# Kernel optimization log

Hardware: AMD Instinct MI355X
Metric: run time of the kernel (lower is better)

Reference implementation:

```python
import jax, jax.numpy as jnp
import numpy as np
from jax.ops import segment_sum

N_NODES = 100_000
N_EDGES = 3_200_000
IN_DIM = 128
HID1, HID2, OUT = 32, 16, 1
N_GRAPHS = 512


def gcn_conv(x, src, dst, W, b, n_nodes):
    """PyG GCNConv: add self-loops, symmetric deg^{-1/2} norm, scatter-add, bias."""
    h = x @ W  # [N, out]
    loop = jnp.arange(n_nodes, dtype=src.dtype)
    s = jnp.concatenate([src, loop])
    d = jnp.concatenate([dst, loop])
    deg = segment_sum(jnp.ones_like(d, dtype=h.dtype), d, num_segments=n_nodes)
    dinv = jax.lax.rsqrt(jnp.maximum(deg, 1.0))  # deg >= 1 due to self-loops
    norm = dinv[s] * dinv[d]  # [E+N]
    msg = h[s] * norm[:, None]  # gather + scale
    out = segment_sum(msg, d, num_segments=n_nodes)  # scatter-add to dst
    return out + b


def setup_inputs() -> dict:
    key = jax.random.key(0)
    ks = jax.random.split(key, 9)
    x = jax.random.normal(ks[0], (N_NODES, IN_DIM), dtype=jnp.float32)
    edge_index = jax.random.randint(ks[1], (2, N_EDGES), 0, N_NODES, dtype=jnp.int64)
    batch = jnp.sort(jax.random.randint(ks[2], (N_NODES,), 0, N_GRAPHS, dtype=jnp.int64))
    W1 = jax.random.normal(ks[3], (IN_DIM, HID1), dtype=jnp.float32) * 0.1
    b1 = jnp.zeros((HID1,), dtype=jnp.float32)
    W2 = jax.random.normal(ks[4], (HID1, HID2), dtype=jnp.float32) * 0.1
    b2 = jnp.zeros((HID2,), dtype=jnp.float32)
    W3 = jax.random.normal(ks[5], (HID2, OUT), dtype=jnp.float32) * 0.1
    b3 = jnp.zeros((OUT,), dtype=jnp.float32)
    return {"x": x, "edge_index": edge_index, "batch": batch,
            "W1": W1, "b1": b1, "W2": W2, "b2": b2, "W3": W3, "b3": b3}


def reference(x, edge_index, batch, W1, b1, W2, b2, W3, b3):
    src, dst = edge_index[0], edge_index[1]
    n = x.shape[0]
    h = jax.nn.relu(gcn_conv(x, src, dst, W1, b1, n))
    h = jax.nn.relu(gcn_conv(h, src, dst, W2, b2, n))
    # global_mean_pool: segment mean over graph ids
    summed = segment_sum(h, batch, num_segments=N_GRAPHS)  # [G, HID2]
    counts = segment_sum(jnp.ones((n,), dtype=h.dtype), batch, num_segments=N_GRAPHS)
    pooled = summed / jnp.maximum(counts, 1.0)[:, None]
    return pooled @ W3 + b3  # [G, 1]
```

## Files before the change

kernel.cpp:

```cpp
#include <hip/hip_runtime.h>
#include <hip/hip_fp16.h>

#define NN 100000
#define NE 3200000
#define NG 512
#define IND 128
#define H1D 32
#define H2D 16
#define BSH 7
#define BN  128
#define NB  782
#define TILE 8192
#define CAP 5120

#define O_DINV   0u
#define O_ROW    100352u
#define O_REND   200704u
#define O_GCUR   301056u
#define O_GSUM   302080u
#define O_M1H    302592u
#define O_M2H    1902592u
#define O_CSRB   2702592u
#define O_CSR    6706432u

__global__ __launch_bounds__(256) void k_init(int* gcur, float* gsum) {
    int i = blockIdx.x * 256 + threadIdx.x;
    if (i < 1024) gcur[i] = i * CAP;
    if (i < NG) gsum[i] = 0.f;
}

__global__ __launch_bounds__(256) void k_binfill(const int* __restrict__ src,
                                                 const int* __restrict__ dst,
                                                 int* __restrict__ gcur,
                                                 unsigned* __restrict__ csrb) {
    __shared__ unsigned se[TILE];
    __shared__ int lc[NB], lofs[NB], lcur[NB], gb[NB];
    __shared__ int sp[256];
    int t = threadIdx.x;
    for (int i = t; i < NB; i += 256) lc[i] = 0;
    __syncthreads();
    int base = blockIdx.x * TILE;
    int end = min(base + TILE, NE);
    int n4 = (end - base) >> 2;
    const int4* dst4 = (const int4*)(dst + base);
    const int4* src4 = (const int4*)(src + base);
    for (int u = t; u < n4; u += 256) {
        int4 v = dst4[u];
        atomicAdd(&lc[v.x >> BSH], 1);
        atomicAdd(&lc[v.y >> BSH], 1);
        atomicAdd(&lc[v.z >> BSH], 1);
        atomicAdd(&lc[v.w >> BSH], 1);
    }
    __syncthreads();
    int b0 = 4 * t;
    int c0 = (b0     < NB) ? lc[b0]     : 0;
    int c1 = (b0 + 1 < NB) ? lc[b0 + 1] : 0;
    int c2 = (b0 + 2 < NB) ? lc[b0 + 2] : 0;
    int c3 = (b0 + 3 < NB) ? lc[b0 + 3] : 0;
    int s4 = c0 + c1 + c2 + c3;
    sp[t] = s4;
    __syncthreads();
    for (int off = 1; off < 256; off <<= 1) {
        int v = (t >= off) ? sp[t - off] : 0;
        __syncthreads();
        sp[t] += v;
        __syncthreads();
    }
    int excl = sp[t] - s4;
    if (b0     < NB) { lofs[b0]     = excl;               lcur[b0]     = excl; }
    if (b0 + 1 < NB) { lofs[b0 + 1] = excl + c0;          lcur[b0 + 1] = excl + c0; }
    if (b0 + 2 < NB) { lofs[b0 + 2] = excl + c0 + c1;     lcur[b0 + 2] = excl + c0 + c1; }
    if (b0 + 3 < NB) { lofs[b0 + 3] = excl + c0 + c1 + c2; lcur[b0 + 3] = excl + c0 + c1 + c2; }
    __syncthreads();
    for (int i = t; i < NB; i += 256) {
        int c = lc[i];
        gb[i] = c ? atomicAdd(&gcur[i], c) : 0;
    }
    __syncthreads();
    for (int u = t; u < n4; u += 256) {
        int4 vd = dst4[u];
        int4 vs = src4[u];
        int b, p;
        b = vd.x >> BSH; p = atomicAdd(&lcur[b], 1);
        se[p] = (unsigned)vs.x | ((unsigned)(vd.x & (BN - 1)) << 17);
        b = vd.y >> BSH; p = atomicAdd(&lcur[b], 1);
        se[p] = (unsigned)vs.y | ((unsigned)(vd.y & (BN - 1)) << 17);
        b = vd.z >> BSH; p = atomicAdd(&lcur[b], 1);
        se[p] = (unsigned)vs.z | ((unsigned)(vd.z & (BN - 1)) << 17);
        b = vd.w >> BSH; p = atomicAdd(&lcur[b], 1);
        se[p] = (unsigned)vs.w | ((unsigned)(vd.w & (BN - 1)) << 17);
    }
    __syncthreads();
    int wv = t >> 6, ln = t & 63;
    for (int b = wv; b < NB; b += 4) {
        int cnt = lc[b];
        int lo = lofs[b], g = gb[b];
        for (int u = ln; u < cnt; u += 64)
            csrb[g + u] = se[lo + u];
    }
}

__global__ __launch_bounds__(256) void k_reorder(const unsigned* __restrict__ csrb,
                                                 const int* __restrict__ gcur,
                                                 int* __restrict__ rowstart,
                                                 int* __restrict__ rowend,
                                                 float* __restrict__ dinv,
                                                 int* __restrict__ csr) {
    __shared__ unsigned se[CAP];
    __shared__ unsigned so[CAP];
    __shared__ int h[BN], cur[BN];
    int t = threadIdx.x;
    int b = blockIdx.x;
    int base = b * CAP;
    int cnt = gcur[b] - base;
    if (t < BN) h[t] = 0;
    __syncthreads();
    for (int i = t; i < cnt; i += 256) {
        unsigned p = csrb[base + i];
        se[i] = p;
        atomicAdd(&h[p >> 17], 1);
    }
    __syncthreads();
    int deg = (t < BN) ? h[t] : 0;
    for (int off = 1; off < BN; off <<= 1) {
        int v = (t < BN && t >= off) ? h[t - off] : 0;
        __syncthreads();
        if (t < BN) h[t] += v;
        __syncthreads();
    }
    int excl = (t < BN) ? (h[t] - deg) : 0;
    if (t < BN) cur[t] = excl;
    int node = (b << BSH) + t;
    if (t < BN && node < NN) {
        rowstart[node] = base + excl;
        rowend[node]   = base + excl + deg;
        dinv[node] = 1.0f / sqrtf((float)(deg + 1));
    }
    __syncthreads();
    for (int i = t; i < cnt; i += 256) {
        unsigned p = se[i];
        int pos = atomicAdd(&cur[p >> 17], 1);
        so[pos] = p;
    }
    __syncthreads();
    for (int i = t; i < cnt; i += 256)
        csr[base + i] = (int)(so[i] & 0x1FFFF);
}

__global__ __launch_bounds__(256) void k_gemm1(const float* __restrict__ x,
                                               const float* __restrict__ W1,
                                               const float* __restrict__ dinv,
                                               __half* __restrict__ m1h) {
    __shared__ float sWt[32 * 132];
    __shared__ float sX[16 * IND];
    int t = threadIdx.x;
    for (int idx = t; idx < IND * H1D; idx += 256) {
        int i = idx >> 5, k = idx & 31;
        sWt[k * 132 + i] = W1[idx];
    }
    const float4* x4 = (const float4*)(x + (size_t)blockIdx.x * 16 * IND);
    ((float4*)sX)[t] = x4[t];
    ((float4*)sX)[t + 256] = x4[t + 256];
    __syncthreads();
    int r = t >> 5, k = t & 31;
    float a0 = 0.f, a1 = 0.f;
#pragma unroll
    for (int i = 0; i < IND; i += 4) {
        float4 w = *(const float4*)&sWt[k * 132 + i];
        float4 p = *(const float4*)&sX[r * IND + i];
        float4 s = *(const float4*)&sX[(r + 8) * IND + i];
        a0 += p.x * w.x + p.y * w.y + p.z * w.z + p.w * w.w;
        a1 += s.x * w.x + s.y * w.y + s.z * w.z + s.w * w.w;
    }
    int n0 = blockIdx.x * 16 + r;
    m1h[(size_t)n0 * 32 + k] = __float2half(a0 * dinv[n0]);
    m1h[(size_t)(n0 + 8) * 32 + k] = __float2half(a1 * dinv[n0 + 8]);
}

__device__ __forceinline__ void h8_acc(const float4& r, float* a) {
    const __half2* h = (const __half2*)&r;
    float2 f0 = __half22float2(h[0]);
    float2 f1 = __half22float2(h[1]);
    float2 f2 = __half22float2(h[2]);
    float2 f3 = __half22float2(h[3]);
    a[0] += f0.x; a[1] += f0.y; a[2] += f1.x; a[3] += f1.y;
    a[4] += f2.x; a[5] += f2.y; a[6] += f3.x; a[7] += f3.y;
}

__global__ __launch_bounds__(256) void k_agg1(const __half* __restrict__ m1h,
                                              const float* __restrict__ dinv,
                                              const int* __restrict__ rowstart,
                                              const int* __restrict__ rowend,
                                              const int* __restrict__ csr,
                                              const float* __restrict__ b1,
                                              const float* __restrict__ W2,
                                              __half* __restrict__ m2h) {
    int t = threadIdx.x;
    int lane = t & 63;
    int j = (lane >> 2) & 7;
    int q = lane & 3;
    int d = (blockIdx.x * 256 + t) >> 5;
    int beg = rowstart[d], end = rowend[d];
    float dv = dinv[d];
    const float4* m4 = (const float4*)m1h;
    float4 selfr = m4[(size_t)d * 4 + q];
    float a[8] = {0.f, 0.f, 0.f, 0.f, 0.f, 0.f, 0.f, 0.f};
    int i = beg + j;
    for (; i + 24 < end; i += 32) {
        int s0 = csr[i], s1 = csr[i + 8], s2 = csr[i + 16], s3 = csr[i + 24];
        float4 A = m4[(size_t)s0 * 4 + q];
        float4 B = m4[(size_t)s1 * 4 + q];
        float4 C = m4[(size_t)s2 * 4 + q];
        float4 D = m4[(size_t)s3 * 4 + q];
        h8_acc(A, a); h8_acc(B, a); h8_acc(C, a); h8_acc(D, a);
    }
    for (; i + 8 < end; i += 16) {
        int s0 = csr[i], s1 = csr[i + 8];
        float4 A = m4[(size_t)s0 * 4 + q];
        float4 B = m4[(size_t)s1 * 4 + q];
        h8_acc(A, a); h8_acc(B, a);
    }
    if (i < end) {
        int s0 = csr[i];
        float4 A = m4[(size_t)s0 * 4 + q];
        h8_acc(A, a);
    }
#pragma unroll
    for (int m = 4; m <= 16; m <<= 1) {
#pragma unroll
        for (int e = 0; e < 8; ++e) a[e] += __shfl_xor(a[e], m);
    }
    float sf[8] = {0.f, 0.f, 0.f, 0.f, 0.f, 0.f, 0.f, 0.f};
    h8_acc(selfr, sf);
    float4 ba = ((const float4*)b1)[q * 2];
    float4 bb = ((const float4*)b1)[q * 2 + 1];
    float bias[8] = {ba.x, ba.y, ba.z, ba.w, bb.x, bb.y, bb.z, bb.w};
    float v[8];
#pragma unroll
    for (int e = 0; e < 8; ++e)
        v[e] = fmaxf((a[e] + sf[e]) * dv + bias[e], 0.f);
    const float2* W2_2 = (const float2*)W2;
    float p0 = 0.f, p1 = 0.f;
#pragma unroll
    for (int e = 0; e < 8; ++e) {
        float2 w = W2_2[(q * 8 + e) * 8 + j];
        p0 += v[e] * w.x;
        p1 += v[e] * w.y;
    }
    p0 += __shfl_xor(p0, 1); p1 += __shfl_xor(p1, 1);
    p0 += __shfl_xor(p0, 2); p1 += __shfl_xor(p1, 2);
    if (q == 0)
        *(__half2*)&m2h[(size_t)d * 16 + 2 * j] = __floats2half2_rn(p0 * dv, p1 * dv);
}

__global__ __launch_bounds__(256) void k_agg2(const __half* __restrict__ m2h,
                                              const float* __restrict__ dinv,
                                              const int* __restrict__ rowstart,
                                              const int* __restrict__ rowend,
                                              const int* __restrict__ csr,
                                              const float* __restrict__ b2,
                                              const float* __restrict__ W3,
                                              const int* __restrict__ batch,
                                              float* __restrict__ gsum) {
    __shared__ float bsum[8];
    __shared__ int   bg[8];
    int t = threadIdx.x;
    int lane = t & 63;
    int j = (lane >> 1) & 15;
    int q = lane & 1;
    int d = (blockIdx.x * 256 + t) >> 5;
    int beg = rowstart[d], end = rowend[d];
    float dv = dinv[d];
    const float4* m4 = (const float4*)m2h;
    float4 selfr = m4[(size_t)d * 2 + q];
    float a[8] = {0.f, 0.f, 0.f, 0.f, 0.f, 0.f, 0.f, 0.f};
    int i = beg + j;
    for (; i + 48 < end; i += 64) {
        int s0 = csr[i], s1 = csr[i + 16], s2 = csr[i + 32], s3 = csr[i + 48];
        float4 A = m4[(size_t)s0 * 2 + q];
        float4 B = m4[(size_t)s1 * 2 + q];
        float4 C = m4[(size_t)s2 * 2 + q];
        float4 D = m4[(size_t)s3 * 2 + q];
        h8_acc(A, a); h8_acc(B, a); h8_acc(C, a); h8_acc(D, a);
    }
    for (; i + 16 < end; i += 32) {
        int s0 = csr[i], s1 = csr[i + 16];
        float4 A = m4[(size_t)s0 * 2 + q];
        float4 B = m4[(size_t)s1 * 2 + q];
        h8_acc(A, a); h8_acc(B, a);
    }
    if (i < end) {
        int s0 = csr[i];
        float4 A = m4[(size_t)s0 * 2 + q];
        h8_acc(A, a);
    }
#pragma unroll
    for (int m = 2; m <= 16; m <<= 1) {
#pragma unroll
        for (int e = 0; e < 8; ++e) a[e] += __shfl_xor(a[e], m);
    }
    float sf[8] = {0.f, 0.f, 0.f, 0.f, 0.f, 0.f, 0.f, 0.f};
    h8_acc(selfr, sf);
    float4 ba = ((const float4*)b2)[q * 2];
    float4 bb = ((const float4*)b2)[q * 2 + 1];
    float4 wa = ((const float4*)W3)[q * 2];
    float4 wb = ((const float4*)W3)[q * 2 + 1];
    float bias[8] = {ba.x, ba.y, ba.z, ba.w, bb.x, bb.y, bb.z, bb.w};
    float w3[8]   = {wa.x, wa.y, wa.z, wa.w, wb.x, wb.y, wb.z, wb.w};
    float partial = 0.f;
#pragma unroll
    for (int e = 0; e < 8; ++e) {
        float v = fmaxf((a[e] + sf[e]) * dv + bias[e], 0.f);
        partial += v * w3[e];
    }
    partial += __shfl_xor(partial, 1);
    int hw = t >> 5;
    if ((lane & 31) == 0) { bg[hw] = batch[d]; bsum[hw] = partial; }
    __syncthreads();
    if (t == 0) {
        float s = bsum[0]; int g = bg[0];
#pragma unroll
        for (int u = 1; u < 8; ++u) {
            if (bg[u] == g) s += bsum[u];
            else { atomicAdd(&gsum[g], s); g = bg[u]; s = bsum[u]; }
        }
        atomicAdd(&gsum[g], s);
    }
}

__global__ __launch_bounds__(256) void k_final(const float* __restrict__ gsum,
                                               const int* __restrict__ batch,
                                               const float* __restrict__ b3,
                                               float* __restrict__ out) {
    int g = blockIdx.x * 256 + threadIdx.x;
    if (g >= NG) return;
    int lo = 0, hi = NN;
    while (lo < hi) { int mid = (lo + hi) >> 1; if (batch[mid] < g) lo = mid + 1; else hi = mid; }
    int lo2 = lo, hi2 = NN;
    while (lo2 < hi2) { int mid = (lo2 + hi2) >> 1; if (batch[mid] < g + 1) lo2 = mid + 1; else hi2 = mid; }
    out[g] = gsum[g] / fmaxf((float)(lo2 - lo), 1.0f) + b3[0];
}

extern "C" void kernel_launch(void* const* d_in, const int* in_sizes, int n_in,
                              void* d_out, int out_size, void* d_ws, size_t ws_size,
                              hipStream_t stream) {
    const float* x     = (const float*)d_in[0];
    const int*   src   = (const int*)d_in[1];
    const int*   dst   = src + NE;
    const int*   batch = (const int*)d_in[2];
    const float* W1 = (const float*)d_in[3];
    const float* b1 = (const float*)d_in[4];
    const float* W2 = (const float*)d_in[5];
    const float* b2 = (const float*)d_in[6];
    const float* W3 = (const float*)d_in[7];
    const float* b3 = (const float*)d_in[8];
    float* out = (float*)d_out;

    float* ws = (float*)d_ws;
    float*    dinv     = ws + O_DINV;
    int*      rowstart = (int*)(ws + O_ROW);
    int*      rowend   = (int*)(ws + O_REND);
    int*      gcur     = (int*)(ws + O_GCUR);
    float*    gsum     = ws + O_GSUM;
    __half*   m1h      = (__half*)(ws + O_M1H);
    __half*   m2h      = (__half*)(ws + O_M2H);
    unsigned* csrb     = (unsigned*)(ws + O_CSRB);
    int*      csr      = (int*)(ws + O_CSR);

    k_init   <<<4, 256, 0, stream>>>(gcur, gsum);
    k_binfill<<<(NE + TILE - 1) / TILE, 256, 0, stream>>>(src, dst, gcur, csrb);
    k_reorder<<<NB, 256, 0, stream>>>(csrb, gcur, rowstart, rowend, dinv, csr);

    k_gemm1  <<<NN / 16, 256, 0, stream>>>(x, W1, dinv, m1h);
    k_agg1   <<<NN / 8, 256, 0, stream>>>(m1h, dinv, rowstart, rowend, csr, b1, W2, m2h);
    k_agg2   <<<NN / 8, 256, 0, stream>>>(m2h, dinv, rowstart, rowend, csr, b2, W3, batch, gsum);
    k_final  <<<2, 256, 0, stream>>>(gsum, batch, b3, out);
}
```

Measured before the change: 324.4 us.

## Merge edge binning and first GEMM into one heterogeneous launch; defer dinv scaling

Edge binning and the x@W1 GEMM now run as two groups of blocks inside a single launch, so the GEMM no longer waits for the degree computation. The dinv scaling of m1h moves into the reorder kernel as an in-place half2 pass. The binning tile stores 16-bit local edge indices in shared memory instead of packed 32-bit entries and re-reads src/dst from global when writing out. The reorder kernel drops its shared staging buffer and reads csrb twice from global. The cost is an extra read-modify-write of m1h and extra global reads in exchange for one fewer launch and cross-stage overlap.

```diff
diff --git a/kernel.cpp b/kernel.cpp
--- a/kernel.cpp
+++ b/kernel.cpp
@@ -11,6 +11,7 @@
 #define BN  128
 #define NB  782
 #define TILE 8192
+#define NBF 391
 #define CAP 5120
 
 #define O_DINV   0u
@@ -29,74 +30,105 @@
     if (i < NG) gsum[i] = 0.f;
 }
 
-__global__ __launch_bounds__(256) void k_binfill(const int* __restrict__ src,
-                                                 const int* __restrict__ dst,
-                                                 int* __restrict__ gcur,
-                                                 unsigned* __restrict__ csrb) {
-    __shared__ unsigned se[TILE];
-    __shared__ int lc[NB], lofs[NB], lcur[NB], gb[NB];
-    __shared__ int sp[256];
+__global__ __launch_bounds__(256) void k_prep1(const int* __restrict__ src,
+                                               const int* __restrict__ dst,
+                                               int* __restrict__ gcur,
+                                               unsigned* __restrict__ csrb,
+                                               const float* __restrict__ x,
+                                               const float* __restrict__ W1,
+                                               __half* __restrict__ m1h) {
+    __shared__ __align__(16) unsigned char smem[30208];
     int t = threadIdx.x;
-    for (int i = t; i < NB; i += 256) lc[i] = 0;
-    __syncthreads();
-    int base = blockIdx.x * TILE;
-    int end = min(base + TILE, NE);
-    int n4 = (end - base) >> 2;
-    const int4* dst4 = (const int4*)(dst + base);
-    const int4* src4 = (const int4*)(src + base);
-    for (int u = t; u < n4; u += 256) {
-        int4 v = dst4[u];
-        atomicAdd(&lc[v.x >> BSH], 1);
-        atomicAdd(&lc[v.y >> BSH], 1);
-        atomicAdd(&lc[v.z >> BSH], 1);
-        atomicAdd(&lc[v.w >> BSH], 1);
-    }
-    __syncthreads();
-    int b0 = 4 * t;
-    int c0 = (b0     < NB) ? lc[b0]     : 0;
-    int c1 = (b0 + 1 < NB) ? lc[b0 + 1] : 0;
-    int c2 = (b0 + 2 < NB) ? lc[b0 + 2] : 0;
-    int c3 = (b0 + 3 < NB) ? lc[b0 + 3] : 0;
-    int s4 = c0 + c1 + c2 + c3;
-    sp[t] = s4;
-    __syncthreads();
-    for (int off = 1; off < 256; off <<= 1) {
-        int v = (t >= off) ? sp[t - off] : 0;
-        __syncthreads();
-        sp[t] += v;
-        __syncthreads();
-    }
-    int excl = sp[t] - s4;
-    if (b0     < NB) { lofs[b0]     = excl;               lcur[b0]     = excl; }
-    if (b0 + 1 < NB) { lofs[b0 + 1] = excl + c0;          lcur[b0 + 1] = excl + c0; }
-    if (b0 + 2 < NB) { lofs[b0 + 2] = excl + c0 + c1;     lcur[b0 + 2] = excl + c0 + c1; }
-    if (b0 + 3 < NB) { lofs[b0 + 3] = excl + c0 + c1 + c2; lcur[b0 + 3] = excl + c0 + c1 + c2; }
-    __syncthreads();
-    for (int i = t; i < NB; i += 256) {
-        int c = lc[i];
-        gb[i] = c ? atomicAdd(&gcur[i], c) : 0;
-    }
-    __syncthreads();
-    for (int u = t; u < n4; u += 256) {
-        int4 vd = dst4[u];
-        int4 vs = src4[u];
-        int b, p;
-        b = vd.x >> BSH; p = atomicAdd(&lcur[b], 1);
-        se[p] = (unsigned)vs.x | ((unsigned)(vd.x & (BN - 1)) << 17);
-        b = vd.y >> BSH; p = atomicAdd(&lcur[b], 1);
-        se[p] = (unsigned)vs.y | ((unsigned)(vd.y & (BN - 1)) << 17);
-        b = vd.z >> BSH; p = atomicAdd(&lcur[b], 1);
-        se[p] = (unsigned)vs.z | ((unsigned)(vd.z & (BN - 1)) << 17);
-        b = vd.w >> BSH; p = atomicAdd(&lcur[b], 1);
-        se[p] = (unsigned)vs.w | ((unsigned)(vd.w & (BN - 1)) << 17);
-    }
-    __syncthreads();
-    int wv = t >> 6, ln = t & 63;
-    for (int b = wv; b < NB; b += 4) {
-        int cnt = lc[b];
-        int lo = lofs[b], g = gb[b];
-        for (int u = ln; u < cnt; u += 64)
-            csrb[g + u] = se[lo + u];
+    if (blockIdx.x < NBF) {
+        unsigned short* se16 = (unsigned short*)smem;
+        int* lc   = (int*)(smem + 16384);
+        int* lofs = (int*)(smem + 19584);
+        int* lcur = (int*)(smem + 22784);
+        int* gb   = (int*)(smem + 25984);
+        int* sp   = (int*)(smem + 29184);
+        for (int i = t; i < NB; i += 256) lc[i] = 0;
+        __syncthreads();
+        int base = blockIdx.x * TILE;
+        int end = min(base + TILE, NE);
+        int n = end - base;
+        int n4 = n >> 2;
+        const int4* dst4 = (const int4*)(dst + base);
+        for (int u = t; u < n4; u += 256) {
+            int4 v = dst4[u];
+            atomicAdd(&lc[v.x >> BSH], 1);
+            atomicAdd(&lc[v.y >> BSH], 1);
+            atomicAdd(&lc[v.z >> BSH], 1);
+            atomicAdd(&lc[v.w >> BSH], 1);
+        }
+        __syncthreads();
+        int b0 = 4 * t;
+        int c0 = (b0     < NB) ? lc[b0]     : 0;
+        int c1 = (b0 + 1 < NB) ? lc[b0 + 1] : 0;
+        int c2 = (b0 + 2 < NB) ? lc[b0 + 2] : 0;
+        int c3 = (b0 + 3 < NB) ? lc[b0 + 3] : 0;
+        int s4 = c0 + c1 + c2 + c3;
+        sp[t] = s4;
+        __syncthreads();
+        for (int off = 1; off < 256; off <<= 1) {
+            int v = (t >= off) ? sp[t - off] : 0;
+            __syncthreads();
+            sp[t] += v;
+            __syncthreads();
+        }
+        int excl = sp[t] - s4;
+        if (b0     < NB) { lofs[b0]     = excl;                lcur[b0]     = excl; }
+        if (b0 + 1 < NB) { lofs[b0 + 1] = excl + c0;           lcur[b0 + 1] = excl + c0; }
+        if (b0 + 2 < NB) { lofs[b0 + 2] = excl + c0 + c1;      lcur[b0 + 2] = excl + c0 + c1; }
+        if (b0 + 3 < NB) { lofs[b0 + 3] = excl + c0 + c1 + c2; lcur[b0 + 3] = excl + c0 + c1 + c2; }
+        __syncthreads();
+        for (int i = t; i < NB; i += 256) {
+            int c = lc[i];
+            gb[i] = c ? atomicAdd(&gcur[i], c) : 0;
+        }
+        __syncthreads();
+        for (int u = t; u < n4; u += 256) {
+            int4 v = dst4[u];
+            int uu = u * 4;
+            int b, p;
+            b = v.x >> BSH; p = atomicAdd(&lcur[b], 1); se16[p] = (unsigned short)(uu);
+            b = v.y >> BSH; p = atomicAdd(&lcur[b], 1); se16[p] = (unsigned short)(uu + 1);
+            b = v.z >> BSH; p = atomicAdd(&lcur[b], 1); se16[p] = (unsigned short)(uu + 2);
+            b = v.w >> BSH; p = atomicAdd(&lcur[b], 1); se16[p] = (unsigned short)(uu + 3);
+        }
+        __syncthreads();
+        for (int i = t; i < n; i += 256) {
+            int u = se16[i];
+            int d = dst[base + u];
+            int s = src[base + u];
+            int b = d >> BSH;
+            int pos = gb[b] + (i - lofs[b]);
+            csrb[pos] = (unsigned)s | ((unsigned)(d & (BN - 1)) << 17);
+        }
+    } else {
+        float* sWt = (float*)smem;
+        float* sX  = (float*)(smem + 16896);
+        int gbk = blockIdx.x - NBF;
+        for (int idx = t; idx < IND * H1D; idx += 256) {
+            int i = idx >> 5, k = idx & 31;
+            sWt[k * 132 + i] = W1[idx];
+        }
+        const float4* x4 = (const float4*)(x + (size_t)gbk * 16 * IND);
+        ((float4*)sX)[t] = x4[t];
+        ((float4*)sX)[t + 256] = x4[t + 256];
+        __syncthreads();
+        int r = t >> 5, k = t & 31;
+        float a0 = 0.f, a1 = 0.f;
+#pragma unroll
+        for (int i = 0; i < IND; i += 4) {
+            float4 w = *(const float4*)&sWt[k * 132 + i];
+            float4 p = *(const float4*)&sX[r * IND + i];
+            float4 s = *(const float4*)&sX[(r + 8) * IND + i];
+            a0 += p.x * w.x + p.y * w.y + p.z * w.z + p.w * w.w;
+            a1 += s.x * w.x + s.y * w.y + s.z * w.z + s.w * w.w;
+        }
+        int n0 = gbk * 16 + r;
+        m1h[(size_t)n0 * 32 + k] = __float2half(a0);
+        m1h[(size_t)(n0 + 8) * 32 + k] = __float2half(a1);
     }
 }
 
@@ -105,21 +137,19 @@
                                                  int* __restrict__ rowstart,
                                                  int* __restrict__ rowend,
                                                  float* __restrict__ dinv,
-                                                 int* __restrict__ csr) {
-    __shared__ unsigned se[CAP];
-    __shared__ unsigned so[CAP];
+                                                 int* __restrict__ csr,
+                                                 __half* __restrict__ m1h) {
+    __shared__ int so[CAP];
     __shared__ int h[BN], cur[BN];
+    __shared__ float sdv[BN];
     int t = threadIdx.x;
     int b = blockIdx.x;
     int base = b * CAP;
     int cnt = gcur[b] - base;
     if (t < BN) h[t] = 0;
     __syncthreads();
-    for (int i = t; i < cnt; i += 256) {
-        unsigned p = csrb[base + i];
-        se[i] = p;
-        atomicAdd(&h[p >> 17], 1);
-    }
+    for (int i = t; i < cnt; i += 256)
+        atomicAdd(&h[csrb[base + i] >> 17], 1);
     __syncthreads();
     int deg = (t < BN) ? h[t] : 0;
     for (int off = 1; off < BN; off <<= 1) {
@@ -131,50 +161,31 @@
     int excl = (t < BN) ? (h[t] - deg) : 0;
     if (t < BN) cur[t] = excl;
     int node = (b << BSH) + t;
-    if (t < BN && node < NN) {
-        rowstart[node] = base + excl;
-        rowend[node]   = base + excl + deg;
-        dinv[node] = 1.0f / sqrtf((float)(deg + 1));
+    if (t < BN) {
+        float dv = 1.0f / sqrtf((float)(deg + 1));
+        sdv[t] = dv;
+        if (node < NN) {
+            rowstart[node] = base + excl;
+            rowend[node]   = base + excl + deg;
+            dinv[node] = dv;
+        }
     }
     __syncthreads();
     for (int i = t; i < cnt; i += 256) {
-        unsigned p = se[i];
+        unsigned p = csrb[base + i];
         int pos = atomicAdd(&cur[p >> 17], 1);
-        so[pos] = p;
+        so[pos] = (int)(p & 0x1FFFF);
     }
     __syncthreads();
     for (int i = t; i < cnt; i += 256)
-        csr[base + i] = (int)(so[i] & 0x1FFFF);
-}
-
-__global__ __launch_bounds__(256) void k_gemm1(const float* __restrict__ x,
-                                               const float* __restrict__ W1,
-                                               const float* __restrict__ dinv,
-                                               __half* __restrict__ m1h) {
-    __shared__ float sWt[32 * 132];
-    __shared__ float sX[16 * IND];
-    int t = threadIdx.x;
-    for (int idx = t; idx < IND * H1D; idx += 256) {
-        int i = idx >> 5, k = idx & 31;
-        sWt[k * 132 + i] = W1[idx];
-    }
-    const float4* x4 = (const float4*)(x + (size_t)blockIdx.x * 16 * IND);
-    ((float4*)sX)[t] = x4[t];
-    ((float4*)sX)[t + 256] = x4[t + 256];
-    __syncthreads();
-    int r = t >> 5, k = t & 31;
-    float a0 = 0.f, a1 = 0.f;
-#pragma unroll
-    for (int i = 0; i < IND; i += 4) {
-        float4 w = *(const float4*)&sWt[k * 132 + i];
-        float4 p = *(const float4*)&sX[r * IND + i];
-        float4 s = *(const float4*)&sX[(r + 8) * IND + i];
-        a0 += p.x * w.x + p.y * w.y + p.z * w.z + p.w * w.w;
-        a1 += s.x * w.x + s.y * w.y + s.z * w.z + s.w * w.w;
-    }
-    int n0 = blockIdx.x * 16 + r;
-    m1h[(size_t)n0 * 32 + k] = __float2half(a0 * dinv[n0]);
-    m1h[(size_t)(n0 + 8) * 32 + k] = __float2half(a1 * dinv[n0 + 8]);
+        csr[base + i] = so[i];
+    int nn = min(BN, NN - (b << BSH));
+    __half2* mrow = (__half2*)(m1h + (size_t)(b << BSH) * 32);
+    for (int idx = t; idx < nn * 16; idx += 256) {
+        float dv = sdv[idx >> 4];
+        float2 f = __half22float2(mrow[idx]);
+        mrow[idx] = __floats2half2_rn(f.x * dv, f.y * dv);
+    }
 }
 
 __device__ __forceinline__ void h8_acc(const float4& r, float* a) {
@@ -368,10 +379,8 @@
     int*      csr      = (int*)(ws + O_CSR);
 
     k_init   <<<4, 256, 0, stream>>>(gcur, gsum);
-    k_binfill<<<(NE + TILE - 1) / TILE, 256, 0, stream>>>(src, dst, gcur, csrb);
-    k_reorder<<<NB, 256, 0, stream>>>(csrb, gcur, rowstart, rowend, dinv, csr);
-
-    k_gemm1  <<<NN / 16, 256, 0, stream>>>(x, W1, dinv, m1h);
+    k_prep1  <<<NBF + NN / 16, 256, 0, stream>>>(src, dst, gcur, csrb, x, W1, m1h);
+    k_reorder<<<NB, 256, 0, stream>>>(csrb, gcur, rowstart, rowend, dinv, csr, m1h);
     k_agg1   <<<NN / 8, 256, 0, stream>>>(m1h, dinv, rowstart, rowend, csr, b1, W2, m2h);
     k_agg2   <<<NN / 8, 256, 0, stream>>>(m2h, dinv, rowstart, rowend, csr, b2, W3, batch, gsum);
     k_final  <<<2, 256, 0, stream>>>(gsum, batch, b3, out);
```

Result: faster. 297.7 us (-8.3%).
